# Optimization experiments

Measured on AMD Instinct MI355X. Metric: run time of the kernel, lower is better.

Reference implementation:

```python
import jax, jax.numpy as jnp
import numpy as np


def _expand_chunk(x):
    # prepend the previous bucket along the chunk axis: [b, nb, bl, ...] -> [b, nb, 2*bl, ...]
    return jnp.concatenate([jnp.roll(x, 1, axis=1), x], axis=2)


def _gather_seq(origin, idx):
    # origin [b, s, d], idx [b, s, r] -> out[b, s, :, r] = origin[b, idx[b, s, r], :]
    b = origin.shape[0]
    g = origin[jnp.arange(b)[:, None, None], idx]  # [b, s, r, d]
    return jnp.transpose(g, (0, 1, 3, 2))          # [b, s, d, r]


def _count_dup_keys(inp, rounds):
    # inp [b, s, K] int32: count duplicate key indices within a window of `rounds` in sorted order
    sort_idx = jnp.argsort(inp, axis=2)
    sorted_k = jnp.take_along_axis(inp, sort_idx, axis=2)
    unsort = jnp.argsort(sort_idx, axis=2)
    cnt = jnp.ones(inp.shape, jnp.float32)
    for i in range(1, rounds):
        eq = (sorted_k[..., i:] == sorted_k[..., :-i]).astype(jnp.float32)
        pad = jnp.zeros(inp.shape[:-1] + (i,), jnp.float32)
        cnt = cnt + jnp.concatenate([pad, eq], axis=-1) + jnp.concatenate([eq, pad], axis=-1)
    return jnp.take_along_axis(cnt, unsort, axis=2)


def setup_inputs() -> dict:
    key = jax.random.key(0)
    k1, k2, k3 = jax.random.split(key, 3)
    B_M_H, SEQ, D_K, N_ROUNDS, N_BUCKETS = 32, 2048, 64, 4, 32
    query = jax.random.normal(k1, (B_M_H, SEQ, D_K), jnp.float32)
    value = jax.random.normal(k2, (B_M_H, SEQ, D_K), jnp.float32)
    rand_matrix = jax.random.normal(k3, (B_M_H, D_K, N_ROUNDS, N_BUCKETS // 2), jnp.float32)
    return {"query": query, "value": value, "rand_matrix": rand_matrix}


def reference(query, value, rand_matrix):
    b, s, d = query.shape
    nr = rand_matrix.shape[2]
    n_buckets = 2 * rand_matrix.shape[3]
    bl = s // n_buckets  # bucket_len

    # --- LSH hashing: argmax over [proj, -proj], then make hashes unique per position ---
    proj = jnp.einsum('bsd,bdrk->bsrk', query, rand_matrix)
    hashes = jnp.argmax(jnp.concatenate([proj, -proj], axis=-1), axis=-1).astype(jnp.int32)
    hashes = hashes * s + jnp.arange(s, dtype=jnp.int32)[None, :, None]  # [b, s, nr]

    sort_idx = jnp.argsort(hashes, axis=1)      # [b, s, nr]
    unsort_idx = jnp.argsort(sort_idx, axis=1)  # [b, s, nr]

    # --- sort queries into buckets ---
    q = _gather_seq(query, sort_idx).reshape(b, n_buckets, bl, d, nr)
    k = _expand_chunk(q)  # [b, nb, 2*bl, d, nr]
    k = k * jax.lax.rsqrt(jnp.maximum(jnp.sum(k * k, axis=-2, keepdims=True), 1e-12))

    qk = jnp.einsum('bnidr,bnjdr->bnijr', q, k) / np.float32(np.sqrt(d))  # [b, nb, bl, 2bl, nr]

    # --- causal / self masks on original positions ---
    qi = sort_idx.reshape(b, n_buckets, bl, nr) % s
    ki = _expand_chunk(qi)  # [b, nb, 2bl, nr]
    mask1 = (qi[:, :, :, None, :] < ki[:, :, None, :, :]).astype(jnp.float32)
    mask2 = (qi[:, :, :, None, :] == ki[:, :, None, :, :]).astype(jnp.float32)
    qk = qk * (1 - mask1) + mask1 * (-1e9)
    qk = qk * (1 - mask2) + mask2 * (-1e5)

    # --- duplicate-key counting across rounds ---
    ki_b = jnp.broadcast_to(ki[:, :, None, :, :], (b, n_buckets, bl, 2 * bl, nr)).reshape(b, s, 2 * bl * nr)
    count_keys = _count_dup_keys(ki_b, nr).reshape(b, s, 2 * bl, nr)

    qk = qk.reshape(b, s, 2 * bl, nr)
    lse = jax.scipy.special.logsumexp(qk, axis=2)  # [b, s, nr]
    sm = jnp.exp(qk - lse[:, :, None, :]) / count_keys

    v = _gather_seq(value, sort_idx).reshape(b, n_buckets, bl, d, nr)
    vk = _expand_chunk(v)  # [b, nb, 2bl, d, nr]
    sm = sm.reshape(b, n_buckets, bl, 2 * bl, nr)
    att = jnp.einsum('bnijr,bnjdr->bnidr', sm, vk).reshape(b, s, d, nr)

    # --- unsort back to original order, per round ---
    att = jnp.transpose(att, (0, 1, 3, 2))  # [b, s, nr, d]
    att = jnp.take_along_axis(att, jnp.broadcast_to(unsort_idx[:, :, :, None], att.shape), axis=1)
    lse = jnp.take_along_axis(lse, unsort_idx, axis=1)

    # --- combine rounds weighted by softmax of logsumexp ---
    w = jax.nn.softmax(lse, axis=-1)  # [b, s, nr]
    return jnp.einsum('bsrd,bsr->bsd', att, w)
```

## Files before the change

### kernel.cpp

```cpp
#include <hip/hip_runtime.h>

typedef unsigned short u16;
typedef unsigned int   u32;
typedef short bf16x8 __attribute__((ext_vector_type(8)));
typedef float f32x16 __attribute__((ext_vector_type(16)));

#define S_  2048
#define D_  64
#define NR_ 4
#define NB_ 32

#define AS 72
#define VS 136
#define PS 136

#define LOG2E 1.44269504088896f
#define LN2   0.69314718055995f

__device__ __forceinline__ float ex2(float x){ return __builtin_amdgcn_exp2f(x); }
__device__ __forceinline__ float frcp(float x){ return __builtin_amdgcn_rcpf(x); }

__device__ __forceinline__ u32 pk2bf(float a, float b){
  u32 r;
  asm("v_cvt_pk_bf16_f32 %0, %1, %2" : "=v"(r) : "v"(a), "v"(b));
  return r;
}
__device__ __forceinline__ void unpack2(u32 w, float &a, float &b){
  a = __uint_as_float(w<<16);
  b = __uint_as_float(w & 0xffff0000u);
}
__device__ __forceinline__ bf16x8 ld8(const u16* p){
  union { uint4 u; bf16x8 v; } x;
  x.u = *(const uint4*)p;
  return x.v;
}

__global__ __launch_bounds__(256, 2) void k_hash(const float* __restrict__ q,
                                                 const float* __restrict__ v,
                                                 const float* __restrict__ R,
                                                 int* __restrict__ hout,
                                                 u16* __restrict__ qb,
                                                 u16* __restrict__ vbuf,
                                                 float* __restrict__ scq){
  __shared__ float Rl[4096];
  int b   = blockIdx.x >> 3;
  int pos = (blockIdx.x & 7) * 256 + threadIdx.x;

  {
    const float4* Rg = (const float4*)(R + (size_t)b * 4096);
    float4* Rs = (float4*)Rl;
    #pragma unroll
    for (int k = 0; k < 4; k++) Rs[k*256 + threadIdx.x] = Rg[k*256 + threadIdx.x];
  }
  __syncthreads();

  const float4* q4 = (const float4*)(q + ((size_t)b * S_ + pos) * D_);
  const float4* v4 = (const float4*)(v + ((size_t)b * S_ + pos) * D_);
  uint2* qw = (uint2*)(qb   + ((size_t)b * S_ + pos) * D_);
  uint2* vw = (uint2*)(vbuf + ((size_t)b * S_ + pos) * D_);

  float acc[64];
  #pragma unroll
  for (int i = 0; i < 64; i++) acc[i] = 0.f;
  float ss = 0.f;

  #pragma unroll 4
  for (int c = 0; c < 16; c++){
    float4 wa = q4[c];
    float4 xa = v4[c];
    ss += wa.x*wa.x + wa.y*wa.y + wa.z*wa.z + wa.w*wa.w;
    qw[c] = make_uint2(pk2bf(wa.x, wa.y), pk2bf(wa.z, wa.w));
    vw[c] = make_uint2(pk2bf(xa.x, xa.y), pk2bf(xa.z, xa.w));
    float qa[4] = {wa.x, wa.y, wa.z, wa.w};
    #pragma unroll
    for (int dd = 0; dd < 4; dd++){
      int d = c * 4 + dd;
      const float4* Rr = (const float4*)(&Rl[d * 64]);
      #pragma unroll
      for (int k4 = 0; k4 < 16; k4++){
        float4 rv = Rr[k4];
        acc[k4*4+0] += qa[dd] * rv.x;
        acc[k4*4+1] += qa[dd] * rv.y;
        acc[k4*4+2] += qa[dd] * rv.z;
        acc[k4*4+3] += qa[dd] * rv.w;
      }
    }
  }
  scq[(size_t)b * S_ + pos] = rsqrtf(fmaxf(ss, 1e-12f)) * 0.125f * LOG2E;

  #pragma unroll
  for (int r = 0; r < 4; r++){
    float bv = acc[r*16]; int bi = 0;
    #pragma unroll
    for (int m = 1; m < 32; m++){
      float vv = (m < 16) ? acc[r*16 + m] : -acc[r*16 + m - 16];
      if (vv > bv){ bv = vv; bi = m; }
    }
    hout[((size_t)b * NR_ + r) * S_ + pos] = bi;
  }
}

__global__ __launch_bounds__(256) void k_sort(const int* __restrict__ h,
                                              int* __restrict__ sidx,
                                              int* __restrict__ chk){
  __shared__ int cnt[32][257];
  __shared__ int base[32];
  int br = blockIdx.x;
  const int* hb = h + (size_t)br * S_;
  int t = threadIdx.x;

  #pragma unroll
  for (int hh = 0; hh < 32; hh++) cnt[hh][t] = 0;
  __syncthreads();

  int hv[8];
  const int4* hb4 = (const int4*)hb;
  int4 a0 = hb4[t*2], a1 = hb4[t*2+1];
  hv[0]=a0.x; hv[1]=a0.y; hv[2]=a0.z; hv[3]=a0.w;
  hv[4]=a1.x; hv[5]=a1.y; hv[6]=a1.z; hv[7]=a1.w;
  #pragma unroll
  for (int k = 0; k < 8; k++) cnt[hv[k]][t]++;
  __syncthreads();

  int wave = t >> 6, lane = t & 63;
  for (int hh = wave*8; hh < wave*8 + 8; hh++){
    int vals[4]; int s0 = 0;
    #pragma unroll
    for (int k = 0; k < 4; k++){ vals[k] = cnt[hh][lane*4+k]; s0 += vals[k]; }
    int incl = s0;
    #pragma unroll
    for (int off = 1; off < 64; off <<= 1){
      int o = __shfl_up(incl, off, 64);
      if (lane >= off) incl += o;
    }
    int run = incl - s0;
    #pragma unroll
    for (int k = 0; k < 4; k++){ int tmp = vals[k]; cnt[hh][lane*4+k] = run; run += tmp; }
    if (lane == 63) base[hh] = incl;
  }
  __syncthreads();
  if (t == 0){
    int run = 0;
    #pragma unroll
    for (int hh = 0; hh < 32; hh++){ int tot = base[hh]; base[hh] = run; run += tot; }
  }
  __syncthreads();

  int p0 = t * 8;
  #pragma unroll
  for (int k = 0; k < 8; k++){
    int hh = hv[k];
    int c = cnt[hh][t];
    int slot = base[hh] + c;
    cnt[hh][t] = c + 1;
    sidx[(size_t)br * S_ + slot]    = p0 + k;
    chk [(size_t)br * S_ + p0 + k]  = slot >> 6;
  }
}

__global__ __launch_bounds__(256, 4) void k_attn(const u16* __restrict__ qb,
                                                 const u16* __restrict__ vb,
                                                 const int* __restrict__ sidx,
                                                 const int* __restrict__ chk,
                                                 const float* __restrict__ scq,
                                                 float* __restrict__ lse_ws,
                                                 u16*  __restrict__ att_ws){
  __shared__ u16 A[128*AS];
  __shared__ u16 SM[64*PS];
  __shared__ int   pkey[128];
  __shared__ float rcnt[128];
  __shared__ float sc[128];
  __shared__ float pm[4*64];
  __shared__ float ps[4*64];

  int blk0 = blockIdx.x;
  int blk  = (blk0 & 7) * 512 + (blk0 >> 3);
  int b = blk >> 7, r = (blk >> 5) & 3, n = blk & 31;
  int npv = (n + 31) & 31;
  int t = threadIdx.x;
  int lane = t & 63, w = t >> 6;
  int la = lane & 31, hh = lane >> 5;
  int coff = hh * 8;
  const int* sb = sidx + ((size_t)b * NR_ + r) * S_;

  int pmine = 0;
  if (t < 128){
    pmine = (t < 64) ? sb[npv*64 + t] : sb[n*64 + (t - 64)];
    pkey[t] = pmine;
  }
  __syncthreads();

  uint4 qk0, qk1, qk2, qk3;
  {
    int row = t >> 1, half = t & 1;
    const uint4* src = (const uint4*)(qb + ((size_t)b*S_ + pkey[row])*D_) + half*4;
    qk0 = src[0]; qk1 = src[1]; qk2 = src[2]; qk3 = src[3];
  }
  int jp = t & 63, dgrp = t >> 6;
  uint4 va0, va1, vb0, vb1;
  {
    const uint4* s0 = (const uint4*)(vb + ((size_t)b*S_ + pkey[2*jp  ])*D_ + dgrp*16);
    const uint4* s1 = (const uint4*)(vb + ((size_t)b*S_ + pkey[2*jp+1])*D_ + dgrp*16);
    va0 = s0[0]; va1 = s0[1]; vb0 = s1[0]; vb1 = s1[1];
  }
  if (t < 128){
    int c = 0;
    #pragma unroll
    for (int rr = 0; rr < 4; rr++){
      int ch = chk[((size_t)b * NR_ + rr) * S_ + pmine];
      c += (ch == n) || (ch == npv);
    }
    if (c < 1) c = 1;
    rcnt[t] = frcp((float)c);
    sc[t] = scq[(size_t)b * S_ + pmine];
  }
  {
    int row = t >> 1, half = t & 1;
    uint4* dst = (uint4*)(&A[row*AS + half*32]);
    dst[0] = qk0; dst[1] = qk1; dst[2] = qk2; dst[3] = qk3;
  }
  __syncthreads();

  float e0[16], e1[16];
  float ml0, ml1;
  {
    int jt = w;
    f32x16 acc0, acc1;
    #pragma unroll
    for (int i = 0; i < 16; i++){ acc0[i] = 0.f; acc1[i] = 0.f; }
    int arow  = (jt*32 + la) * AS;
    int brow0 = (64 + la) * AS;
    int brow1 = (96 + la) * AS;
    __builtin_amdgcn_s_setprio(1);
    #pragma unroll
    for (int ks = 0; ks < 4; ks++){
      int o = ks*16 + coff;
      bf16x8 af = ld8(&A[arow  + o]);
      bf16x8 b0 = ld8(&A[brow0 + o]);
      bf16x8 b1 = ld8(&A[brow1 + o]);
      acc0 = __builtin_amdgcn_mfma_f32_32x32x16_bf16(af, b0, acc0, 0, 0, 0);
      acc1 = __builtin_amdgcn_mfma_f32_32x32x16_bf16(af, b1, acc1, 0, 0, 0);
    }
    __builtin_amdgcn_s_setprio(0);
    int pj[16]; float scj[16];
    #pragma unroll
    for (int g = 0; g < 4; g++){
      int j0 = jt*32 + g*8 + 4*hh;
      int4   pv  = *(const int4*)(&pkey[j0]);
      float4 sv  = *(const float4*)(&sc[j0]);
      pj[g*4+0]=pv.x; pj[g*4+1]=pv.y; pj[g*4+2]=pv.z; pj[g*4+3]=pv.w;
      scj[g*4+0]=sv.x; scj[g*4+1]=sv.y; scj[g*4+2]=sv.z; scj[g*4+3]=sv.w;
    }
    int pi0 = pkey[64 + la], pi1 = pkey[96 + la];
    float x0[16], x1[16];
    #pragma unroll
    for (int reg = 0; reg < 16; reg++){
      float a0v = acc0[reg] * scj[reg];
      float a1v = acc1[reg] * scj[reg];
      if (pi0 < pj[reg]) a0v = -1442695040.0f; else if (pi0 == pj[reg]) a0v = -144269.504f;
      if (pi1 < pj[reg]) a1v = -1442695040.0f; else if (pi1 == pj[reg]) a1v = -144269.504f;
      x0[reg] = a0v; x1[reg] = a1v;
    }
    {
      float u0 = fmaxf(fmaxf(x0[0],x0[1]), fmaxf(x0[2],x0[3]));
      float u1 = fmaxf(fmaxf(x0[4],x0[5]), fmaxf(x0[6],x0[7]));
      float u2 = fmaxf(fmaxf(x0[8],x0[9]), fmaxf(x0[10],x0[11]));
      float u3 = fmaxf(fmaxf(x0[12],x0[13]), fmaxf(x0[14],x0[15]));
      ml0 = fmaxf(fmaxf(u0,u1), fmaxf(u2,u3));
      float w0 = fmaxf(fmaxf(x1[0],x1[1]), fmaxf(x1[2],x1[3]));
      float w1 = fmaxf(fmaxf(x1[4],x1[5]), fmaxf(x1[6],x1[7]));
      float w2 = fmaxf(fmaxf(x1[8],x1[9]), fmaxf(x1[10],x1[11]));
      float w3 = fmaxf(fmaxf(x1[12],x1[13]), fmaxf(x1[14],x1[15]));
      ml1 = fmaxf(fmaxf(w0,w1), fmaxf(w2,w3));
    }
    #pragma unroll
    for (int reg = 0; reg < 16; reg++){
      e0[reg] = ex2(x0[reg] - ml0);
      e1[reg] = ex2(x1[reg] - ml1);
    }
    float s0, s1;
    {
      float u0 = (e0[0]+e0[1])+(e0[2]+e0[3]);
      float u1 = (e0[4]+e0[5])+(e0[6]+e0[7]);
      float u2 = (e0[8]+e0[9])+(e0[10]+e0[11]);
      float u3 = (e0[12]+e0[13])+(e0[14]+e0[15]);
      s0 = (u0+u1)+(u2+u3);
      float w0 = (e1[0]+e1[1])+(e1[2]+e1[3]);
      float w1 = (e1[4]+e1[5])+(e1[6]+e1[7]);
      float w2 = (e1[8]+e1[9])+(e1[10]+e1[11]);
      float w3 = (e1[12]+e1[13])+(e1[14]+e1[15]);
      s1 = (w0+w1)+(w2+w3);
    }
    float om0 = __shfl_xor(ml0, 32, 64), os0 = __shfl_xor(s0, 32, 64);
    float om1 = __shfl_xor(ml1, 32, 64), os1 = __shfl_xor(s1, 32, 64);
    float m20 = fmaxf(ml0, om0);
    float m21 = fmaxf(ml1, om1);
    float s20 = s0 * ex2(ml0 - m20) + os0 * ex2(om0 - m20);
    float s21 = s1 * ex2(ml1 - m21) + os1 * ex2(om1 - m21);
    if (hh == 0){
      pm[jt*64 + la]      = m20;  ps[jt*64 + la]      = s20;
      pm[jt*64 + 32 + la] = m21;  ps[jt*64 + 32 + la] = s21;
    }
  }
  __syncthreads();

  {
    int jt = w;
    float mg0 = pm[la],      mg1 = pm[32 + la];
    #pragma unroll
    for (int k = 1; k < 4; k++){
      mg0 = fmaxf(mg0, pm[k*64 + la]);
      mg1 = fmaxf(mg1, pm[k*64 + 32 + la]);
    }
    float sg0 = 0.f, sg1 = 0.f;
    #pragma unroll
    for (int k = 0; k < 4; k++){
      sg0 += ps[k*64 + la]      * ex2(pm[k*64 + la]      - mg0);
      sg1 += ps[k*64 + 32 + la] * ex2(pm[k*64 + 32 + la] - mg1);
    }
    float f0 = ex2(ml0 - mg0) * frcp(sg0);
    float f1 = ex2(ml1 - mg1) * frcp(sg1);
    #pragma unroll
    for (int g = 0; g < 4; g++){
      int j0 = jt*32 + g*8 + 4*hh;
      float4 rc = *(const float4*)(&rcnt[j0]);
      float p00 = e0[g*4+0]*f0*rc.x, p01 = e0[g*4+1]*f0*rc.y;
      float p02 = e0[g*4+2]*f0*rc.z, p03 = e0[g*4+3]*f0*rc.w;
      float p10 = e1[g*4+0]*f1*rc.x, p11 = e1[g*4+1]*f1*rc.y;
      float p12 = e1[g*4+2]*f1*rc.z, p13 = e1[g*4+3]*f1*rc.w;
      *(uint2*)(&SM[la*PS + j0])        = make_uint2(pk2bf(p00,p01), pk2bf(p02,p03));
      *(uint2*)(&SM[(32+la)*PS + j0])   = make_uint2(pk2bf(p10,p11), pk2bf(p12,p13));
    }
    if (w == 0 && hh == 0){
      lse_ws[((size_t)b*S_ + pkey[64 + la])*NR_ + r] = mg0 * LN2 + __logf(sg0);
      lse_ws[((size_t)b*S_ + pkey[96 + la])*NR_ + r] = mg1 * LN2 + __logf(sg1);
    }
  }
  {
    u32 au[8] = {va0.x, va0.y, va0.z, va0.w, va1.x, va1.y, va1.z, va1.w};
    u32 bu[8] = {vb0.x, vb0.y, vb0.z, vb0.w, vb1.x, vb1.y, vb1.z, vb1.w};
    u32* vtp = (u32*)A;
    #pragma unroll
    for (int k = 0; k < 8; k++){
      int d0 = dgrp*16 + 2*k;
      u32 even = (au[k] & 0xffffu) | (bu[k] << 16);
      u32 odd  = (au[k] >> 16)     | (bu[k] & 0xffff0000u);
      vtp[ d0      * (VS/2) + jp] = even;
      vtp[(d0 + 1) * (VS/2) + jp] = odd;
    }
  }
  __syncthreads();

  {
    int Mt2 = w >> 1, Nt2 = w & 1;
    f32x16 acc;
    #pragma unroll
    for (int i = 0; i < 16; i++) acc[i] = 0.f;
    int arow = (Mt2*32 + la) * VS;
    int brow = (Nt2*32 + la) * PS;
    __builtin_amdgcn_s_setprio(1);
    #pragma unroll
    for (int ks = 0; ks < 8; ks++){
      int o = ks*16 + coff;
      bf16x8 af = ld8(&A[arow + o]);
      bf16x8 bf = ld8(&SM[brow + o]);
      acc = __builtin_amdgcn_mfma_f32_32x32x16_bf16(af, bf, acc, 0, 0, 0);
    }
    __builtin_amdgcn_s_setprio(0);
    int i = Nt2*32 + la;
    int p = pkey[64 + i];
    u16* base = att_ws + (((size_t)b*S_ + p)*NR_ + r)*D_ + Mt2*32 + 4*hh;
    #pragma unroll
    for (int g = 0; g < 4; g++){
      uint2 val = make_uint2(pk2bf(acc[4*g+0], acc[4*g+1]),
                             pk2bf(acc[4*g+2], acc[4*g+3]));
      *(uint2*)(base + g*8) = val;
    }
  }
}

__global__ __launch_bounds__(256) void k_comb(const float* __restrict__ lse_ws,
                                              const u16* __restrict__ att_ws,
                                              float* __restrict__ out){
  size_t idx4 = (size_t)blockIdx.x * 256 + threadIdx.x;
  size_t pd = idx4 >> 4;
  int d0 = (int)(idx4 & 15) * 4;
  float4 lv = *(const float4*)(lse_ws + pd * 4);
  float m = fmaxf(fmaxf(lv.x, lv.y), fmaxf(lv.z, lv.w));
  float e0 = __expf(lv.x - m), e1 = __expf(lv.y - m);
  float e2 = __expf(lv.z - m), e3 = __expf(lv.w - m);
  float inv = frcp(e0 + e1 + e2 + e3);
  e0 *= inv; e1 *= inv; e2 *= inv; e3 *= inv;
  const u16* a = att_ws + pd * 256 + d0;
  uint2 u0 = *(const uint2*)(a);
  uint2 u1 = *(const uint2*)(a + 64);
  uint2 u2 = *(const uint2*)(a + 128);
  uint2 u3 = *(const uint2*)(a + 192);
  float4 o;
  float a0,b0,a1,b1,a2,b2,a3,b3;
  unpack2(u0.x,a0,b0); unpack2(u1.x,a1,b1); unpack2(u2.x,a2,b2); unpack2(u3.x,a3,b3);
  o.x = a0*e0 + a1*e1 + a2*e2 + a3*e3;
  o.y = b0*e0 + b1*e1 + b2*e2 + b3*e3;
  unpack2(u0.y,a0,b0); unpack2(u1.y,a1,b1); unpack2(u2.y,a2,b2); unpack2(u3.y,a3,b3);
  o.z = a0*e0 + a1*e1 + a2*e2 + a3*e3;
  o.w = b0*e0 + b1*e1 + b2*e2 + b3*e3;
  *(float4*)(out + pd * D_ + d0) = o;
}

extern "C" void kernel_launch(void* const* d_in, const int* in_sizes, int n_in,
                              void* d_out, int out_size, void* d_ws, size_t ws_size,
                              hipStream_t stream){
  const float* q = (const float*)d_in[0];
  const float* v = (const float*)d_in[1];
  const float* R = (const float*)d_in[2];

  char* w = (char*)d_ws;
  int*   h    = (int*)  (w + 0);
  int*   sidx = (int*)  (w + (size_t)(1u << 20));
  int*   chkA = (int*)  (w + (size_t)(2u << 20));
  float* lse  = (float*)(w + (size_t)(3u << 20));
  u16*   att  = (u16*)  (w + (size_t)(4u << 20));
  u16*   qb   = (u16*)  (w + (size_t)(36u << 20));
  u16*   vbuf = (u16*)  (w + (size_t)(44u << 20));
  float* scq  = (float*)(w + (size_t)(52u << 20));
  float* out  = (float*)d_out;

  k_hash <<<256,  256, 0, stream>>>(q, v, R, h, qb, vbuf, scq);
  k_sort <<<128,  256, 0, stream>>>(h, sidx, chkA);
  k_attn <<<4096, 256, 0, stream>>>(qb, vbuf, sidx, chkA, scq, lse, att);
  k_comb <<<4096, 256, 0, stream>>>(lse, att, out);
}
```

Baseline: 147.4 us.

## Store attention output in sorted order and unsort via gather in combine

The attention kernel used to scatter each output row straight to its original sequence position, which meant scattered 8-byte writes. It now stages the tile in shared memory and writes contiguous 128-byte rows in sorted order using nontemporal stores. The sort kernel now keeps the full slot index so the combine kernel can look up each round's sorted slot and gather from it. This moves the random access from the writes to the reads in the combine kernel and adds an extra barrier plus an LDS round trip.

```diff
diff --git a/kernel.cpp b/kernel.cpp
--- a/kernel.cpp
+++ b/kernel.cpp
@@ -4,6 +4,7 @@
 typedef unsigned int   u32;
 typedef short bf16x8 __attribute__((ext_vector_type(8)));
 typedef float f32x16 __attribute__((ext_vector_type(16)));
+typedef unsigned int u32x4v __attribute__((ext_vector_type(4)));
 
 #define S_  2048
 #define D_  64
@@ -13,6 +14,7 @@
 #define AS 72
 #define VS 136
 #define PS 136
+#define OS 72
 
 #define LOG2E 1.44269504088896f
 #define LN2   0.69314718055995f
@@ -33,6 +35,10 @@
   union { uint4 u; bf16x8 v; } x;
   x.u = *(const uint4*)p;
   return x.v;
+}
+__device__ __forceinline__ void nt_store16(u16* p, uint4 v){
+  u32x4v x; x.x = v.x; x.y = v.y; x.z = v.z; x.w = v.w;
+  __builtin_nontemporal_store(x, (u32x4v*)p);
 }
 
 __global__ __launch_bounds__(256, 2) void k_hash(const float* __restrict__ q,
@@ -154,7 +160,7 @@
     int slot = base[hh] + c;
     cnt[hh][t] = c + 1;
     sidx[(size_t)br * S_ + slot]    = p0 + k;
-    chk [(size_t)br * S_ + p0 + k]  = slot >> 6;
+    chk [(size_t)br * S_ + p0 + k]  = slot;
   }
 }
 
@@ -207,7 +213,7 @@
     int c = 0;
     #pragma unroll
     for (int rr = 0; rr < 4; rr++){
-      int ch = chk[((size_t)b * NR_ + rr) * S_ + pmine];
+      int ch = chk[((size_t)b * NR_ + rr) * S_ + pmine] >> 6;
       c += (ch == n) || (ch == npv);
     }
     if (c < 1) c = 1;
@@ -367,35 +373,50 @@
       acc = __builtin_amdgcn_mfma_f32_32x32x16_bf16(af, bf, acc, 0, 0, 0);
     }
     __builtin_amdgcn_s_setprio(0);
+    __syncthreads();
     int i = Nt2*32 + la;
-    int p = pkey[64 + i];
-    u16* base = att_ws + (((size_t)b*S_ + p)*NR_ + r)*D_ + Mt2*32 + 4*hh;
+    int dbase = Mt2*32 + 4*hh;
     #pragma unroll
     for (int g = 0; g < 4; g++){
-      uint2 val = make_uint2(pk2bf(acc[4*g+0], acc[4*g+1]),
-                             pk2bf(acc[4*g+2], acc[4*g+3]));
-      *(uint2*)(base + g*8) = val;
-    }
+      *(uint2*)(&SM[i*OS + dbase + g*8]) =
+          make_uint2(pk2bf(acc[4*g+0], acc[4*g+1]),
+                     pk2bf(acc[4*g+2], acc[4*g+3]));
+    }
+  }
+  __syncthreads();
+  {
+    int i2 = t >> 2, qd = t & 3;
+    uint4 x0 = *(const uint4*)(&SM[i2*OS + qd*16]);
+    uint4 x1 = *(const uint4*)(&SM[i2*OS + qd*16 + 8]);
+    u16* dst = att_ws + (((size_t)b*NR_ + r)*S_ + n*64 + i2)*(size_t)D_ + qd*16;
+    nt_store16(dst,     x0);
+    nt_store16(dst + 8, x1);
   }
 }
 
 __global__ __launch_bounds__(256) void k_comb(const float* __restrict__ lse_ws,
+                                              const int* __restrict__ chk,
                                               const u16* __restrict__ att_ws,
                                               float* __restrict__ out){
   size_t idx4 = (size_t)blockIdx.x * 256 + threadIdx.x;
   size_t pd = idx4 >> 4;
   int d0 = (int)(idx4 & 15) * 4;
+  int b = (int)(pd >> 11);
+  int p = (int)(pd & (S_ - 1));
   float4 lv = *(const float4*)(lse_ws + pd * 4);
   float m = fmaxf(fmaxf(lv.x, lv.y), fmaxf(lv.z, lv.w));
   float e0 = __expf(lv.x - m), e1 = __expf(lv.y - m);
   float e2 = __expf(lv.z - m), e3 = __expf(lv.w - m);
   float inv = frcp(e0 + e1 + e2 + e3);
   e0 *= inv; e1 *= inv; e2 *= inv; e3 *= inv;
-  const u16* a = att_ws + pd * 256 + d0;
-  uint2 u0 = *(const uint2*)(a);
-  uint2 u1 = *(const uint2*)(a + 64);
-  uint2 u2 = *(const uint2*)(a + 128);
-  uint2 u3 = *(const uint2*)(a + 192);
+  int s0 = chk[((size_t)b*NR_ + 0)*S_ + p];
+  int s1 = chk[((size_t)b*NR_ + 1)*S_ + p];
+  int s2 = chk[((size_t)b*NR_ + 2)*S_ + p];
+  int s3 = chk[((size_t)b*NR_ + 3)*S_ + p];
+  uint2 u0 = *(const uint2*)(att_ws + (((size_t)b*NR_ + 0)*S_ + s0)*(size_t)D_ + d0);
+  uint2 u1 = *(const uint2*)(att_ws + (((size_t)b*NR_ + 1)*S_ + s1)*(size_t)D_ + d0);
+  uint2 u2 = *(const uint2*)(att_ws + (((size_t)b*NR_ + 2)*S_ + s2)*(size_t)D_ + d0);
+  uint2 u3 = *(const uint2*)(att_ws + (((size_t)b*NR_ + 3)*S_ + s3)*(size_t)D_ + d0);
   float4 o;
   float a0,b0,a1,b1,a2,b2,a3,b3;
   unpack2(u0.x,a0,b0); unpack2(u1.x,a1,b1); unpack2(u2.x,a2,b2); unpack2(u3.x,a3,b3);
@@ -428,5 +449,5 @@
   k_hash <<<256,  256, 0, stream>>>(q, v, R, h, qb, vbuf, scq);
   k_sort <<<128,  256, 0, stream>>>(h, sidx, chkA);
   k_attn <<<4096, 256, 0, stream>>>(qb, vbuf, sidx, chkA, scq, lse, att);
-  k_comb <<<4096, 256, 0, stream>>>(lse, att, out);
-}
+  k_comb <<<4096, 256, 0, stream>>>(lse, chkA, att, out);
+}
```

Measured after the change: 142.3 us. -3.5%, faster.
